# Kernel tuning notes

Hardware: AMD Instinct MI355X
Metric: run time of the kernel (lower is better)

The kernel has to match this reference:

```python
import jax, jax.numpy as jnp
import numpy as np

B, C, H, W = 8, 256, 64, 64
S = 2            # area_size = sqrt(num_areas)
A = S * S        # num_areas
NH = 8           # num_heads (hardcoded in module)
EPS = 1e-5       # nn.LayerNorm default eps


def setup_inputs() -> dict:
    key = jax.random.key(0)
    ks = jax.random.split(key, 4)
    scale = 0.02
    return {
        "x": jax.random.normal(ks[0], (B, C, H, W), jnp.float32),
        "W_in": jax.random.normal(ks[1], (A, 3 * C, C), jnp.float32) * scale,
        "b_in": jnp.zeros((A, 3 * C), jnp.float32),
        "W_out": jax.random.normal(ks[2], (A, C, C), jnp.float32) * scale,
        "b_out": jnp.zeros((A, C), jnp.float32),
        "gamma": jnp.ones((C,), jnp.float32),
        "beta": jnp.zeros((C,), jnp.float32),
    }


def reference(x, W_in, b_in, W_out, b_out, gamma, beta):
    b, c, h, w = x.shape
    ah, aw = h // S, w // S
    L = ah * aw
    dh = c // NH

    # split into 2x2 areas, flatten each to a sequence: [B, A, L, C]
    # area index = i*S + j (row-major), matching the torch loop order
    xa = (x.reshape(b, c, S, ah, S, aw)
            .transpose(0, 2, 4, 3, 5, 1)   # [B, i, j, ah, aw, C]
            .reshape(b, A, L, c))

    # per-area in-projection (torch Linear: y = x @ W^T + b)
    qkv = jnp.einsum('balc,adc->bald', xa, W_in) + b_in[None, :, None, :]
    q, k, v = jnp.split(qkv, 3, axis=-1)
    q = q.reshape(b, A, L, NH, dh)
    k = k.reshape(b, A, L, NH, dh)
    v = v.reshape(b, A, L, NH, dh)

    scale = jnp.asarray(dh, x.dtype) ** -0.5
    scores = jnp.einsum('balhd,bamhd->bahlm', q * scale, k)  # [B,A,NH,L,L]
    attn = jax.nn.softmax(scores, axis=-1)
    o = jnp.einsum('bahlm,bamhd->balhd', attn, v).reshape(b, A, L, c)
    o = jnp.einsum('balc,adc->bald', o, W_out) + b_out[None, :, None, :]

    # residual + shared LayerNorm over channel dim
    y = o + xa
    mu = jnp.mean(y, axis=-1, keepdims=True)
    var = jnp.mean((y - mu) ** 2, axis=-1, keepdims=True)
    y = (y - mu) * jax.lax.rsqrt(var + EPS) * gamma + beta

    # reassemble areas back to [B, C, H, W]
    out = (y.reshape(b, S, S, ah, aw, c)
             .transpose(0, 5, 1, 3, 2, 4)  # [B, C, i, ah, j, aw]
             .reshape(b, c, h, w))
    return out
```

## Files before the change

### kernel.cpp

```cpp
#include <hip/hip_runtime.h>
#include <cstdint>
#include <cstddef>

#define B_    8
#define C_    256
#define H_    64
#define W_    64
#define A_    4
#define NH_   8
#define DH_   32
#define L_    1024
#define NPAIR 32
#define QKVN  768

typedef __bf16 bf16;
typedef __bf16 bf16x8 __attribute__((ext_vector_type(8)));
typedef __bf16 bf16x4 __attribute__((ext_vector_type(4)));
typedef float  f32x4  __attribute__((ext_vector_type(4)));

#define QSCALE 0.25506866729736328f

__device__ inline f32x4 mfma16(bf16x8 a, bf16x8 b, f32x4 c) {
    return __builtin_amdgcn_mfma_f32_16x16x32_bf16(a, b, c, 0, 0, 0);
}
__device__ inline bf16x8 ld8(const bf16* p) { return *(const bf16x8*)p; }

__device__ inline void stage16(const bf16* g, bf16* l) {
    __builtin_amdgcn_global_load_lds(
        (const __attribute__((address_space(1))) void*)g,
        (__attribute__((address_space(3))) void*)l, 16, 0, 0);
}

#define NW4 (786432 / 4)
#define NO4 (262144 / 4)
__global__ __launch_bounds__(256) void k_split(const float* __restrict__ x,
                                               bf16* __restrict__ xa,
                                               const float* __restrict__ Win,
                                               const float* __restrict__ Wout,
                                               bf16* __restrict__ Winb,
                                               bf16* __restrict__ Woutb) {
    __shared__ float lds[32][257];
    int bid = blockIdx.x;
    int t = threadIdx.x;
    if (bid >= NPAIR * 32) {
        int tid = (bid - NPAIR * 32) * 256 + t;
        if (tid < NW4) {
            float4 v = ((const float4*)Win)[tid];
            bf16x4 ov = {(bf16)v.x, (bf16)v.y, (bf16)v.z, (bf16)v.w};
            ((bf16x4*)Winb)[tid] = ov;
        } else if (tid < NW4 + NO4) {
            int t2 = tid - NW4;
            float4 v = ((const float4*)Wout)[t2];
            bf16x4 ov = {(bf16)v.x, (bf16)v.y, (bf16)v.z, (bf16)v.w};
            ((bf16x4*)Woutb)[t2] = ov;
        }
        return;
    }
    int pair = bid >> 5, p = bid & 31;
    int b = pair >> 2, a = pair & 3, i = a >> 1, j = a & 1;
    int q = t & 31, csub = t >> 5;
    const float* xb = x + (size_t)b * C_ * H_ * W_ + (size_t)(i * 32 + p) * W_ + j * 32;
    for (int r = 0; r < 32; ++r) {
        int c = r * 8 + csub;
        lds[q][c] = xb[(size_t)c * H_ * W_ + q];
    }
    __syncthreads();
    bf16* xr = xa + ((size_t)pair * L_ + (size_t)p * 32) * C_;
    for (int r = 0; r < 32; ++r) {
        xr[(size_t)r * C_ + t] = (bf16)lds[r][t];
    }
}

__global__ __launch_bounds__(256) void k_qkv(const bf16* __restrict__ xa,
                                             const bf16* __restrict__ Win,
                                             const float* __restrict__ bin,
                                             bf16* __restrict__ qk,
                                             bf16* __restrict__ vT) {
    __shared__ __align__(16) bf16 lA[128 * 64];
    __shared__ __align__(16) bf16 lB[128 * 64];
    int bid = blockIdx.x;
    int nt = bid % 6, mt = (bid / 6) & 7, pair = bid / 48;
    int a = pair & 3;
    int t = threadIdx.x, w = t >> 6, lane = t & 63;
    int wm = w >> 1, wn = w & 1;
    int quad = lane >> 4, l16 = lane & 15;
    int m0 = mt * 128, n0 = nt * 128;
    int r8 = lane >> 3, pc = lane & 7, jj = pc ^ r8;
    const bf16* ga = xa + (size_t)pair * L_ * C_ + (size_t)(m0 + w * 32 + r8) * C_ + jj * 8;
    const bf16* gb = Win + (size_t)a * QKVN * C_ + (size_t)(n0 + w * 32 + r8) * C_ + jj * 8;
    f32x4 acc[4][4];
#pragma unroll
    for (int fm = 0; fm < 4; ++fm)
#pragma unroll
        for (int fn = 0; fn < 4; ++fn) acc[fm][fn] = (f32x4){0.f, 0.f, 0.f, 0.f};
    for (int k0 = 0; k0 < C_; k0 += 64) {
        __syncthreads();
#pragma unroll
        for (int i = 0; i < 4; ++i) {
            stage16(ga + (size_t)(i * 8) * C_ + k0, lA + (w * 32 + i * 8) * 64);
            stage16(gb + (size_t)(i * 8) * C_ + k0, lB + (w * 32 + i * 8) * 64);
        }
        __syncthreads();
#pragma unroll
        for (int ks = 0; ks < 2; ++ks) {
            int p = (ks * 4 + quad) ^ (l16 & 7);
            bf16x8 am[4], bn[4];
#pragma unroll
            for (int f = 0; f < 4; ++f) {
                am[f] = *(const bf16x8*)&lA[(wm * 64 + f * 16 + l16) * 64 + p * 8];
                bn[f] = *(const bf16x8*)&lB[(wn * 64 + f * 16 + l16) * 64 + p * 8];
            }
#pragma unroll
            for (int fm = 0; fm < 4; ++fm)
#pragma unroll
                for (int fn = 0; fn < 4; ++fn)
                    acc[fm][fn] = mfma16(am[fm], bn[fn], acc[fm][fn]);
        }
    }
    int colbase = n0 + wn * 64;
    int mb = m0 + wm * 64;
    if (colbase < 512) {
        float sc = (colbase < 256) ? QSCALE : 1.0f;
        bf16* ob = qk + (size_t)pair * L_ * 512;
#pragma unroll
        for (int fn = 0; fn < 4; ++fn) {
            int col = colbase + fn * 16 + l16;
            float bias = bin[a * QKVN + col];
#pragma unroll
            for (int fm = 0; fm < 4; ++fm) {
                int m = mb + fm * 16 + quad * 4;
#pragma unroll
                for (int r = 0; r < 4; ++r)
                    ob[(size_t)(m + r) * 512 + col] = (bf16)((acc[fm][fn][r] + bias) * sc);
            }
        }
    } else {
        bf16* vb = vT + (size_t)pair * C_ * L_;
#pragma unroll
        for (int fn = 0; fn < 4; ++fn) {
            int e = colbase - 512 + fn * 16 + l16;
            float bias = bin[a * QKVN + colbase + fn * 16 + l16];
#pragma unroll
            for (int fm = 0; fm < 4; ++fm) {
                int m = mb + fm * 16 + quad * 4;
                bf16x4 pk = {(bf16)(acc[fm][fn][0] + bias), (bf16)(acc[fm][fn][1] + bias),
                             (bf16)(acc[fm][fn][2] + bias), (bf16)(acc[fm][fn][3] + bias)};
                *(bf16x4*)&vb[(size_t)e * L_ + m] = pk;
            }
        }
    }
}

__global__ __launch_bounds__(256) void k_attn(const bf16* __restrict__ qk,
                                              const bf16* __restrict__ vT,
                                              bf16* __restrict__ o) {
    __shared__ __align__(16) bf16 pl[4][1024];
    __shared__ __align__(16) bf16 klds[4 * 512];
    __shared__ __align__(16) bf16 vlds[4 * 512];
    int bid = blockIdx.x;
    int pair = bid & 31, rest = bid >> 5;
    int head = rest & 7, qb = rest >> 3;
    int t = threadIdx.x, w = t >> 6, lane = t & 63, quad = lane >> 4, l16 = lane & 15;
    const bf16* qbp = qk + (size_t)pair * L_ * 512;
    const bf16* kg = qbp + (size_t)(l16 * 4 + w) * 512 + 256 + head * DH_ + quad * 8;
    const bf16* vg = vT + ((size_t)pair * C_ + head * DH_ + (w & 1) * 16 + l16) * L_
                        + (w >> 1) * 32 + quad * 8;
    bf16* kdst = &klds[w * 512];
    bf16* vdst = &vlds[w * 512];
    int qbase = qb * 128 + w * 32;
    bf16x8 qf[2];
    f32x4 acc0[2], acc1[2], l4[2];
#pragma unroll
    for (int f = 0; f < 2; ++f) {
        qf[f] = ld8(qbp + (size_t)(qbase + f * 16 + l16) * 512 + head * DH_ + quad * 8);
        acc0[f] = (f32x4){0.f, 0.f, 0.f, 0.f};
        acc1[f] = (f32x4){0.f, 0.f, 0.f, 0.f};
        l4[f]   = (f32x4){0.f, 0.f, 0.f, 0.f};
    }
    stage16(kg, kdst);
    stage16(vg, vdst);
    __syncthreads();

    for (int kv0 = 0; kv0 < L_; kv0 += 64) {
        bf16x8 kf[4], vf[4];
#pragma unroll
        for (int i = 0; i < 4; ++i) {
            kf[i] = ld8(&klds[(i * 64 + lane) * 8]);
            vf[i] = ld8(&vlds[(i * 64 + lane) * 8]);
        }
        __syncthreads();
        int kvn = (kv0 + 64) & (L_ - 1);
        stage16(kg + (size_t)kvn * 512, kdst);
        stage16(vg + kvn, vdst);
#pragma unroll
        for (int f = 0; f < 2; ++f) {
            f32x4 s[4];
#pragma unroll
            for (int kb = 0; kb < 4; ++kb) s[kb] = mfma16(qf[f], kf[kb], (f32x4){0.f, 0.f, 0.f, 0.f});
            char* pw = (char*)&pl[w][0];
#pragma unroll
            for (int r = 0; r < 4; ++r) {
                float p0 = __builtin_amdgcn_exp2f(s[0][r]);
                float p1 = __builtin_amdgcn_exp2f(s[1][r]);
                float p2 = __builtin_amdgcn_exp2f(s[2][r]);
                float p3 = __builtin_amdgcn_exp2f(s[3][r]);
                l4[f][r] += (p0 + p1) + (p2 + p3);
                bf16x4 pv = {(bf16)p0, (bf16)p1, (bf16)p2, (bf16)p3};
                int row = quad * 4 + r;
                int wo = (row * 128 + l16 * 8) ^ ((row & 7) << 4);
                *(bf16x4*)(pw + wo) = pv;
            }
#pragma unroll
            for (int ks = 0; ks < 2; ++ks) {
                int ro = (l16 * 128 + ks * 64 + quad * 16) ^ ((l16 & 7) << 4);
                bf16x8 pf = *(const bf16x8*)(pw + ro);
                acc0[f] = mfma16(pf, vf[ks * 2 + 0], acc0[f]);
                acc1[f] = mfma16(pf, vf[ks * 2 + 1], acc1[f]);
            }
        }
        __syncthreads();
    }
    bf16* orow = o + (size_t)pair * L_ * C_ + head * DH_;
#pragma unroll
    for (int f = 0; f < 2; ++f) {
#pragma unroll
        for (int r = 0; r < 4; ++r) {
            float s1 = l4[f][r];
#pragma unroll
            for (int off = 1; off < 16; off <<= 1) s1 += __shfl_xor(s1, off);
            float inv = 1.f / s1;
            int row = qbase + f * 16 + quad * 4 + r;
            orow[(size_t)row * C_ + l16]      = (bf16)(acc0[f][r] * inv);
            orow[(size_t)row * C_ + 16 + l16] = (bf16)(acc1[f][r] * inv);
        }
    }
}

__global__ __launch_bounds__(256) void k_out(const bf16* __restrict__ o,
                                             const bf16* __restrict__ Wout,
                                             const float* __restrict__ bout,
                                             const bf16* __restrict__ xa,
                                             const float* __restrict__ gamma,
                                             const float* __restrict__ beta,
                                             float* __restrict__ out) {
    __shared__ __align__(16) char smem[49152];
    bf16* lA = (bf16*)smem;
    bf16* lB = (bf16*)(smem + 16384);
    float* tr = (float*)smem;
    __shared__ float red[2][2][64][2];
    int bid = blockIdx.x;
    int mt = bid & 7, pair = bid >> 3;
    int a = pair & 3;
    int t = threadIdx.x, w = t >> 6, lane = t & 63;
    int wm = w >> 1, wn = w & 1;
    int quad = lane >> 4, l16 = lane & 15;
    int m0 = mt * 128;
    int r8 = lane >> 3, pc = lane & 7, jj = pc ^ r8;
    const bf16* ga = o + (size_t)pair * L_ * C_ + (size_t)(m0 + w * 32 + r8) * C_ + jj * 8;
    const bf16* gb = Wout + (size_t)a * C_ * C_ + (size_t)(w * 64 + r8) * C_ + jj * 8;
    f32x4 acc[4][8];
#pragma unroll
    for (int fm = 0; fm < 4; ++fm)
#pragma unroll
        for (int fn = 0; fn < 8; ++fn) acc[fm][fn] = (f32x4){0.f, 0.f, 0.f, 0.f};
    for (int k0 = 0; k0 < C_; k0 += 64) {
        __syncthreads();
#pragma unroll
        for (int i = 0; i < 4; ++i)
            stage16(ga + (size_t)(i * 8) * C_ + k0, lA + (w * 32 + i * 8) * 64);
#pragma unroll
        for (int i = 0; i < 8; ++i)
            stage16(gb + (size_t)(i * 8) * C_ + k0, lB + (w * 64 + i * 8) * 64);
        __syncthreads();
#pragma unroll
        for (int ks = 0; ks < 2; ++ks) {
            int p = (ks * 4 + quad) ^ (l16 & 7);
            bf16x8 am[4], bn[8];
#pragma unroll
            for (int f = 0; f < 4; ++f)
                am[f] = *(const bf16x8*)&lA[(wm * 64 + f * 16 + l16) * 64 + p * 8];
#pragma unroll
            for (int f = 0; f < 8; ++f)
                bn[f] = *(const bf16x8*)&lB[(wn * 128 + f * 16 + l16) * 64 + p * 8];
#pragma unroll
            for (int fm = 0; fm < 4; ++fm)
#pragma unroll
                for (int fn = 0; fn < 8; ++fn)
                    acc[fm][fn] = mfma16(am[fm], bn[fn], acc[fm][fn]);
        }
    }
    const bf16* xb = xa + ((size_t)pair * L_ + m0 + wm * 64) * C_;
    float g8[8], be8[8];
#pragma unroll
    for (int fn = 0; fn < 8; ++fn) {
        int col = wn * 128 + fn * 16 + l16;
        float bias = bout[a * C_ + col];
        g8[fn] = gamma[col];
        be8[fn] = beta[col];
#pragma unroll
        for (int fm = 0; fm < 4; ++fm)
#pragma unroll
            for (int r = 0; r < 4; ++r)
                acc[fm][fn][r] += bias + (float)xb[(size_t)(fm * 16 + quad * 4 + r) * C_ + col];
    }
#pragma unroll
    for (int fm = 0; fm < 4; ++fm) {
#pragma unroll
        for (int r = 0; r < 4; ++r) {
            float s1 = 0.f, s2 = 0.f;
#pragma unroll
            for (int fn = 0; fn < 8; ++fn) {
                float v = acc[fm][fn][r];
                s1 += v; s2 += v * v;
            }
#pragma unroll
            for (int off = 1; off < 16; off <<= 1) {
                s1 += __shfl_xor(s1, off);
                s2 += __shfl_xor(s2, off);
            }
            if (l16 == 0) {
                int rl = fm * 16 + quad * 4 + r;
                red[wm][wn][rl][0] = s1;
                red[wm][wn][rl][1] = s2;
            }
        }
    }
    __syncthreads();
#pragma unroll
    for (int fm = 0; fm < 4; ++fm) {
#pragma unroll
        for (int r = 0; r < 4; ++r) {
            int rl = fm * 16 + quad * 4 + r;
            float t1 = red[wm][0][rl][0] + red[wm][1][rl][0];
            float t2 = red[wm][0][rl][1] + red[wm][1][rl][1];
            float mu = t1 * (1.f / 256.f);
            float var = t2 * (1.f / 256.f) - mu * mu;
            float rstd = rsqrtf(var + 1e-5f);
#pragma unroll
            for (int fn = 0; fn < 8; ++fn)
                acc[fm][fn][r] = (acc[fm][fn][r] - mu) * rstd * g8[fn] + be8[fn];
        }
    }
    int b = pair >> 2, i = (a >> 1), j = a & 1;
    int q = t & 31, csub = t >> 5;
    float* ob = out + (size_t)b * C_ * H_ * W_ + (size_t)(i * 32 + (m0 >> 5)) * W_ + j * 32;
#pragma unroll
    for (int ch = 0; ch < 4; ++ch) {
        __syncthreads();
        if (wm == (ch >> 1)) {
#pragma unroll
            for (int k = 0; k < 2; ++k) {
                int fm = (ch & 1) * 2 + k;
                int rb = (fm & 1) * 16 + quad * 4;
#pragma unroll
                for (int r = 0; r < 4; ++r)
#pragma unroll
                    for (int fn = 0; fn < 8; ++fn)
                        tr[(rb + r) * 258 + wn * 128 + fn * 16 + l16] = acc[fm][fn][r];
            }
        }
        __syncthreads();
#pragma unroll
        for (int r32 = 0; r32 < 32; ++r32) {
            int c = r32 * 8 + csub;
            ob[(size_t)c * (H_ * W_) + (size_t)ch * W_ + q] = tr[q * 258 + c];
        }
    }
}

extern "C" void kernel_launch(void* const* d_in, const int* in_sizes, int n_in,
                              void* d_out, int out_size, void* d_ws, size_t ws_size,
                              hipStream_t stream) {
    (void)in_sizes; (void)n_in; (void)out_size; (void)ws_size;
    const float* x     = (const float*)d_in[0];
    const float* Win   = (const float*)d_in[1];
    const float* bin   = (const float*)d_in[2];
    const float* Wout  = (const float*)d_in[3];
    const float* bout  = (const float*)d_in[4];
    const float* gamma = (const float*)d_in[5];
    const float* beta  = (const float*)d_in[6];
    float* out = (float*)d_out;

    char* ws = (char*)d_ws;
    bf16* xa    = (bf16*)ws;
    bf16* qk    = (bf16*)(ws + ((size_t)16 << 20));
    bf16* vT    = (bf16*)(ws + ((size_t)48 << 20));
    bf16* o     = (bf16*)(ws + ((size_t)64 << 20));
    bf16* Winb  = (bf16*)(ws + ((size_t)80 << 20));
    bf16* Woutb = (bf16*)(ws + ((size_t)82 << 20));

    k_split<<<NPAIR * 32 + 1024, 256, 0, stream>>>(x, xa, Win, Wout, Winb, Woutb);
    k_qkv<<<NPAIR * 8 * 6, 256, 0, stream>>>(xa, Winb, bin, qk, vT);
    k_attn<<<NPAIR * NH_ * 8, 256, 0, stream>>>(qk, vT, o);
    k_out<<<NPAIR * 8, 256, 0, stream>>>(o, Woutb, bout, xa, gamma, beta, out);
}
```

Before: 206.0 us.

## Stage QKV epilogue through LDS for coalesced stores; compute softmax row sums via MFMA

The QKV GEMM epilogue now writes bias-added bf16 results into a padded per-wave LDS slab and then issues 16-byte row-contiguous global stores for both the Q/K and transposed V outputs. This replaces scattered 2-byte and 8-byte stores. In the attention kernel, the softmax denominator is now accumulated by an extra MFMA against a ones vector using the bf16-rounded probabilities, replacing per-element fp32 adds and the final cross-lane shuffle reduction. The cost is an extra sync and LDS traffic in the epilogue, plus one more MFMA per PV step. The row sum also changes slightly because it now uses bf16-rounded values.

```diff
diff --git a/kernel.cpp b/kernel.cpp
--- a/kernel.cpp
+++ b/kernel.cpp
@@ -76,8 +76,9 @@
                                              const float* __restrict__ bin,
                                              bf16* __restrict__ qk,
                                              bf16* __restrict__ vT) {
-    __shared__ __align__(16) bf16 lA[128 * 64];
-    __shared__ __align__(16) bf16 lB[128 * 64];
+    __shared__ __align__(16) char smem[32768];
+    bf16* lA = (bf16*)smem;
+    bf16* lB = (bf16*)(smem + 16384);
     int bid = blockIdx.x;
     int nt = bid % 6, mt = (bid / 6) & 7, pair = bid / 48;
     int a = pair & 3;
@@ -119,33 +120,54 @@
     }
     int colbase = n0 + wn * 64;
     int mb = m0 + wm * 64;
+    __syncthreads();
+    bf16* slab = (bf16*)smem + w * 2304;
+    float bias[4];
+#pragma unroll
+    for (int fn = 0; fn < 4; ++fn) bias[fn] = bin[a * QKVN + colbase + fn * 16 + l16];
+    int sr = lane >> 3, seg = lane & 7;
     if (colbase < 512) {
         float sc = (colbase < 256) ? QSCALE : 1.0f;
         bf16* ob = qk + (size_t)pair * L_ * 512;
 #pragma unroll
-        for (int fn = 0; fn < 4; ++fn) {
-            int col = colbase + fn * 16 + l16;
-            float bias = bin[a * QKVN + col];
-#pragma unroll
-            for (int fm = 0; fm < 4; ++fm) {
-                int m = mb + fm * 16 + quad * 4;
-#pragma unroll
-                for (int r = 0; r < 4; ++r)
-                    ob[(size_t)(m + r) * 512 + col] = (bf16)((acc[fm][fn][r] + bias) * sc);
+        for (int pass = 0; pass < 2; ++pass) {
+#pragma unroll
+            for (int k = 0; k < 2; ++k) {
+                int fm = pass * 2 + k;
+#pragma unroll
+                for (int fn = 0; fn < 4; ++fn)
+#pragma unroll
+                    for (int r = 0; r < 4; ++r)
+                        slab[(k * 16 + quad * 4 + r) * 72 + fn * 16 + l16] =
+                            (bf16)((acc[fm][fn][r] + bias[fn]) * sc);
+            }
+#pragma unroll
+            for (int rr = 0; rr < 4; ++rr) {
+                int row = rr * 8 + sr;
+                bf16x8 v = *(const bf16x8*)&slab[row * 72 + seg * 8];
+                *(bf16x8*)&ob[(size_t)(mb + pass * 32 + row) * 512 + colbase + seg * 8] = v;
             }
         }
     } else {
         bf16* vb = vT + (size_t)pair * C_ * L_;
-#pragma unroll
-        for (int fn = 0; fn < 4; ++fn) {
-            int e = colbase - 512 + fn * 16 + l16;
-            float bias = bin[a * QKVN + colbase + fn * 16 + l16];
-#pragma unroll
-            for (int fm = 0; fm < 4; ++fm) {
-                int m = mb + fm * 16 + quad * 4;
-                bf16x4 pk = {(bf16)(acc[fm][fn][0] + bias), (bf16)(acc[fm][fn][1] + bias),
-                             (bf16)(acc[fm][fn][2] + bias), (bf16)(acc[fm][fn][3] + bias)};
-                *(bf16x4*)&vb[(size_t)e * L_ + m] = pk;
+        int e00 = colbase - 512;
+#pragma unroll
+        for (int pass = 0; pass < 2; ++pass) {
+#pragma unroll
+            for (int k = 0; k < 2; ++k) {
+                int fn = pass * 2 + k;
+#pragma unroll
+                for (int fm = 0; fm < 4; ++fm) {
+                    bf16x4 pk = {(bf16)(acc[fm][fn][0] + bias[fn]), (bf16)(acc[fm][fn][1] + bias[fn]),
+                                 (bf16)(acc[fm][fn][2] + bias[fn]), (bf16)(acc[fm][fn][3] + bias[fn])};
+                    *(bf16x4*)&slab[(k * 16 + l16) * 72 + fm * 16 + quad * 4] = pk;
+                }
+            }
+#pragma unroll
+            for (int rr = 0; rr < 4; ++rr) {
+                int el = rr * 8 + sr;
+                bf16x8 v = *(const bf16x8*)&slab[el * 72 + seg * 8];
+                *(bf16x8*)&vb[(size_t)(e00 + pass * 32 + el) * L_ + mb + seg * 8] = v;
             }
         }
     }
@@ -168,14 +190,16 @@
     bf16* kdst = &klds[w * 512];
     bf16* vdst = &vlds[w * 512];
     int qbase = qb * 128 + w * 32;
+    const bf16x8 ones = {(bf16)1.f, (bf16)1.f, (bf16)1.f, (bf16)1.f,
+                         (bf16)1.f, (bf16)1.f, (bf16)1.f, (bf16)1.f};
     bf16x8 qf[2];
-    f32x4 acc0[2], acc1[2], l4[2];
+    f32x4 acc0[2], acc1[2], accS[2];
 #pragma unroll
     for (int f = 0; f < 2; ++f) {
         qf[f] = ld8(qbp + (size_t)(qbase + f * 16 + l16) * 512 + head * DH_ + quad * 8);
         acc0[f] = (f32x4){0.f, 0.f, 0.f, 0.f};
         acc1[f] = (f32x4){0.f, 0.f, 0.f, 0.f};
-        l4[f]   = (f32x4){0.f, 0.f, 0.f, 0.f};
+        accS[f] = (f32x4){0.f, 0.f, 0.f, 0.f};
     }
     stage16(kg, kdst);
     stage16(vg, vdst);
@@ -204,7 +228,6 @@
                 float p1 = __builtin_amdgcn_exp2f(s[1][r]);
                 float p2 = __builtin_amdgcn_exp2f(s[2][r]);
                 float p3 = __builtin_amdgcn_exp2f(s[3][r]);
-                l4[f][r] += (p0 + p1) + (p2 + p3);
                 bf16x4 pv = {(bf16)p0, (bf16)p1, (bf16)p2, (bf16)p3};
                 int row = quad * 4 + r;
                 int wo = (row * 128 + l16 * 8) ^ ((row & 7) << 4);
@@ -216,6 +239,7 @@
                 bf16x8 pf = *(const bf16x8*)(pw + ro);
                 acc0[f] = mfma16(pf, vf[ks * 2 + 0], acc0[f]);
                 acc1[f] = mfma16(pf, vf[ks * 2 + 1], acc1[f]);
+                accS[f] = mfma16(pf, ones, accS[f]);
             }
         }
         __syncthreads();
@@ -225,10 +249,7 @@
     for (int f = 0; f < 2; ++f) {
 #pragma unroll
         for (int r = 0; r < 4; ++r) {
-            float s1 = l4[f][r];
-#pragma unroll
-            for (int off = 1; off < 16; off <<= 1) s1 += __shfl_xor(s1, off);
-            float inv = 1.f / s1;
+            float inv = 1.f / accS[f][r];
             int row = qbase + f * 16 + quad * 4 + r;
             orow[(size_t)row * C_ + l16]      = (bf16)(acc0[f][r] * inv);
             orow[(size_t)row * C_ + 16 + l16] = (bf16)(acc1[f][r] * inv);
```

Result: slower. 210.4 us (+2.2%).
